# Performance work log

Hardware: AMD Instinct MI355X
Metric: run time of the kernel (lower is better)

The kernel has to match this reference:

```python
import jax, jax.numpy as jnp
import numpy as np
import math

D = 2048
N1 = 250  # fixed by fc1 = Linear(250, 1)
N2 = 27   # fixed by fc2 = Linear(27, 1) for img_size=96


def setup_inputs() -> dict:
    key = jax.random.key(0)
    ks = jax.random.split(key, 18)
    s = 0.02
    def w(k, shape):
        return jax.random.normal(k, shape, dtype=jnp.float32) * s
    return {
        "input_tensor1": jax.random.normal(ks[0], (N1, D), dtype=jnp.float32),
        "input_tensor2": jax.random.normal(ks[1], (N2, D), dtype=jnp.float32),
        "Wq1": w(ks[2], (D, D)), "bq1": jnp.zeros((D,), jnp.float32),
        "Wk1": w(ks[3], (D, D)), "bk1": jnp.zeros((D,), jnp.float32),
        "Wv1": w(ks[4], (D, D)), "bv1": jnp.zeros((D,), jnp.float32),
        "Wq2": w(ks[5], (D, D)), "bq2": jnp.zeros((D,), jnp.float32),
        "Wk2": w(ks[6], (D, D)), "bk2": jnp.zeros((D,), jnp.float32),
        "Wv2": w(ks[7], (D, D)), "bv2": jnp.zeros((D,), jnp.float32),
        "w_fc1": w(ks[8], (N1,)), "b_fc1": jnp.zeros((), jnp.float32),
        "w_fc2": w(ks[9], (N2,)), "b_fc2": jnp.zeros((), jnp.float32),
    }


def reference(input_tensor1, input_tensor2,
              Wq1, bq1, Wk1, bk1, Wv1, bv1,
              Wq2, bq2, Wk2, bk2, Wv2, bv2,
              w_fc1, b_fc1, w_fc2, b_fc2):
    d = input_tensor1.shape[1]
    q1 = input_tensor1 @ Wq1.T + bq1  # [N1, D]
    k1 = input_tensor1 @ Wk1.T + bk1
    v1 = input_tensor1 @ Wv1.T + bv1
    q2 = input_tensor2 @ Wq2.T + bq2  # [N2, D]
    k2 = input_tensor2 @ Wk2.T + bk2
    v2 = input_tensor2 @ Wv2.T + bv2
    scale = 1.0 / math.sqrt(d)

    # sigmoid cross-attention scores
    probs1 = jax.nn.sigmoid((q2 @ k1.T) * scale)  # [N2, N1]
    probs2 = jax.nn.sigmoid((q1 @ k2.T) * scale)  # [N1, N2]

    # Original builds whole[t, i, d] = probs1[t, i] * v2[t, d] then applies
    # fc1 (Linear(N1,1)) along i: ctx1[t,d] = v2[t,d] * (probs1[t,:] @ w_fc1) + b_fc1.
    # Fused form avoids the [N2, N1, D] intermediate; math identical.
    context_layer1 = v2 * (probs1 @ w_fc1)[:, None] + b_fc1  # [N2, D]
    context_layer2 = v1 * (probs2 @ w_fc2)[:, None] + b_fc2  # [N1, D]

    return (context_layer2, probs2, context_layer1, probs1)
```

## Files before the change

kernel.cpp:

```cpp
#include <hip/hip_runtime.h>

typedef unsigned short u16;
typedef unsigned int u32;
typedef __attribute__((ext_vector_type(8))) short short8;
typedef __attribute__((ext_vector_type(4))) float f32x4;

#define DD 2048
constexpr int OFF_P2   = 512000;
constexpr int OFF_CTX1 = 518750;
constexpr int OFF_P1   = 574046;

constexpr int SLB = 512000;
constexpr int SLS = 55296;
constexpr int Q1P = 0;
constexpr int K1P = 1024000;
constexpr int V1P = 2048000;
constexpr int Q2P = 3072000;
constexpr int K2P = Q2P + 4*SLS;
constexpr int V2P = K2P + 4*SLS;
constexpr int S1P = V2P + 4*SLS;
constexpr int S2P = S1P + 8*8192;
constexpr int G1A = S2P + 8*8192;

__device__ __forceinline__ u16 f2bf(float f){
  u32 u = __float_as_uint(f);
  u += 0x7fffu + ((u >> 16) & 1u);
  return (u16)(u >> 16);
}
__device__ __forceinline__ u32 pk(float a, float b){
  return (u32)f2bf(a) | ((u32)f2bf(b) << 16);
}

struct P6 { const float* W[6]; const float* b[6]; };

__global__ __launch_bounds__(256) void k6nt(
    const float* __restrict__ in1, const float* __restrict__ in2,
    P6 par, float* __restrict__ ws)
{
  __shared__ u16 lds_a[64*72];
  __shared__ u16 lds_b[64*72];
  const int b = blockIdx.x, t = threadIdx.x;
  const float* A; int Mreal, m0, n0, kbase, KT, g; float* outp;
  if (b < 768){
    g = b >> 8; int r = b & 255;
    m0 = (r >> 6) * 64; int r2 = r & 63; n0 = (r2 >> 1) * 64; int ks = r2 & 1;
    A = in1; Mreal = 250; kbase = ks * 1024; KT = 16;
    outp = ws + g * (2*SLB) + ks * SLB;
  } else {
    int s = b - 768; g = 3 + s / 128; int r = s % 128;
    n0 = (r >> 2) * 64; int ks = r & 3;
    A = in2; Mreal = 27; m0 = 0; kbase = ks * 512; KT = 8;
    outp = ws + Q2P + (g - 3) * (4*SLS) + ks * SLS;
  }
  const bool addb = (kbase == 0);
  const float* Bw = par.W[g];
  const float* bias = par.b[g];

  const int w = t>>6, l = t&63, wm = w>>1, wn = w&1;
  const int srow = t>>4, scol = (t&15)*4;
  float4 pfa[4], pfb[4];

  auto loadt = [&](int k0){
#pragma unroll
    for (int p=0;p<4;p++){
      int row = p*16 + srow;
      int gm = m0 + row;
      if (gm < Mreal) pfa[p] = *(const float4*)&A[(size_t)gm*DD + k0 + scol];
      else { pfa[p].x=0.f; pfa[p].y=0.f; pfa[p].z=0.f; pfa[p].w=0.f; }
      pfb[p] = *(const float4*)&Bw[(size_t)(n0+row)*DD + k0 + scol];
    }
  };

  f32x4 acc[2][2];
#pragma unroll
  for (int i=0;i<2;i++)
#pragma unroll
    for (int j=0;j<2;j++) acc[i][j] = (f32x4){0.f,0.f,0.f,0.f};

  loadt(kbase);
#pragma unroll 1
  for (int kt=0; kt<KT; ++kt){
    __syncthreads();
#pragma unroll
    for (int p=0;p<4;p++){
      int row = p*16 + srow;
      uint2 av; av.x = pk(pfa[p].x, pfa[p].y); av.y = pk(pfa[p].z, pfa[p].w);
      *(uint2*)&lds_a[row*72 + scol] = av;
      uint2 bw; bw.x = pk(pfb[p].x, pfb[p].y); bw.y = pk(pfb[p].z, pfb[p].w);
      *(uint2*)&lds_b[row*72 + scol] = bw;
    }
    __syncthreads();
    if (kt < KT-1) loadt(kbase + (kt+1)*64);
#pragma unroll
    for (int kk=0; kk<2; ++kk){
      const int kf = kk*32 + (l>>4)*8;
      short8 af[2], bfr[2];
#pragma unroll
      for (int mf=0;mf<2;mf++) af[mf]  = *(const short8*)&lds_a[(wm*32+mf*16+(l&15))*72 + kf];
#pragma unroll
      for (int nf=0;nf<2;nf++) bfr[nf] = *(const short8*)&lds_b[(wn*32+nf*16+(l&15))*72 + kf];
#pragma unroll
      for (int mf=0;mf<2;mf++)
#pragma unroll
        for (int nf=0;nf<2;nf++)
          acc[mf][nf] = __builtin_amdgcn_mfma_f32_16x16x32_bf16(af[mf], bfr[nf], acc[mf][nf], 0, 0, 0);
    }
  }
#pragma unroll
  for (int mf=0;mf<2;mf++)
#pragma unroll
    for (int nf=0;nf<2;nf++){
      int colg = n0 + wn*32 + nf*16 + (l&15);
      float bv = addb ? bias[colg] : 0.f;
#pragma unroll
      for (int r=0;r<4;r++){
        int m = m0 + wm*32 + mf*16 + ((l>>4)<<2) + r;
        if (m < Mreal) outp[(size_t)m*DD + colg] = acc[mf][nf][r] + bv;
      }
    }
}

__global__ __launch_bounds__(256) void kS(float* __restrict__ ws)
{
  __shared__ u16 lds_a[32*72];
  __shared__ u16 lds_b[64*72];
  const int b = blockIdx.x, t = threadIdx.x;
  const int mat = b>>5, r = b&31, jt = r>>3, ks = r&7;
  const int j0 = jt*64, kbase = ks*256;
  const float* Ap = ws + (mat ? K2P : Q2P);
  const float* Bp = ws + (mat ? Q1P : K1P);
  float* OUT = ws + (mat ? S2P : S1P) + ks*8192;
  const int w = t>>6, l = t&63, wm = w>>1, wn = w&1;
  f32x4 acc[2];
  acc[0] = (f32x4){0.f,0.f,0.f,0.f};
  acc[1] = (f32x4){0.f,0.f,0.f,0.f};
#pragma unroll 1
  for (int kt=0; kt<4; ++kt){
    const int kc = kbase + kt*64;
    __syncthreads();
#pragma unroll
    for (int p=0;p<2;p++){
      int f4i = p*256 + t, row = f4i>>4, c4 = (f4i&15)*4;
      float4 v; v.x=0.f; v.y=0.f; v.z=0.f; v.w=0.f;
      if (row < 27){
        const float* base = Ap + (size_t)row*DD + kc + c4;
        float4 v0 = *(const float4*)(base);
        float4 v1 = *(const float4*)(base + SLS);
        float4 v2 = *(const float4*)(base + 2*SLS);
        float4 v3 = *(const float4*)(base + 3*SLS);
        v.x = (v0.x+v1.x)+(v2.x+v3.x); v.y = (v0.y+v1.y)+(v2.y+v3.y);
        v.z = (v0.z+v1.z)+(v2.z+v3.z); v.w = (v0.w+v1.w)+(v2.w+v3.w);
      }
      uint2 pv; pv.x = pk(v.x, v.y); pv.y = pk(v.z, v.w);
      *(uint2*)&lds_a[row*72 + c4] = pv;
    }
#pragma unroll
    for (int p=0;p<4;p++){
      int f4i = p*256 + t, row = f4i>>4, c4 = (f4i&15)*4;
      int j = j0 + row;
      float4 v; v.x=0.f; v.y=0.f; v.z=0.f; v.w=0.f;
      if (j < 250){
        const float* base = Bp + (size_t)j*DD + kc + c4;
        float4 v0 = *(const float4*)(base);
        float4 v1 = *(const float4*)(base + SLB);
        v.x = v0.x+v1.x; v.y = v0.y+v1.y; v.z = v0.z+v1.z; v.w = v0.w+v1.w;
      }
      uint2 pv; pv.x = pk(v.x, v.y); pv.y = pk(v.z, v.w);
      *(uint2*)&lds_b[row*72 + c4] = pv;
    }
    __syncthreads();
#pragma unroll
    for (int kk=0; kk<2; ++kk){
      const int kf = kk*32 + (l>>4)*8;
      short8 af = *(const short8*)&lds_a[(wm*16+(l&15))*72 + kf];
#pragma unroll
      for (int nf=0;nf<2;nf++){
        short8 bfr = *(const short8*)&lds_b[(wn*32+nf*16+(l&15))*72 + kf];
        acc[nf] = __builtin_amdgcn_mfma_f32_16x16x32_bf16(af, bfr, acc[nf], 0, 0, 0);
      }
    }
  }
#pragma unroll
  for (int nf=0;nf<2;nf++){
    int col = j0 + wn*32 + nf*16 + (l&15);
#pragma unroll
    for (int rr=0;rr<4;rr++){
      int row = wm*16 + ((l>>4)<<2) + rr;
      OUT[row*256 + col] = acc[nf][rr];
    }
  }
}

__global__ __launch_bounds__(256) void k_finish(
    const float* __restrict__ ws,
    const float* __restrict__ w_fc1, const float* __restrict__ w_fc2,
    const float* __restrict__ b_fc1p, const float* __restrict__ b_fc2p,
    float* __restrict__ g1acc, float* __restrict__ d_out)
{
  const int b = blockIdx.x, t = threadIdx.x, w = t>>6, l = t&63;
  const int j = b*4 + w;
  if (j >= 250) return;
  const float scale = 0.022097086912079608f;
  float gv = 0.f;
  if (l < 27){
    const float* S1p = ws + S1P;
    const float* S2p = ws + S2P;
    float s1 = 0.f, s2 = 0.f;
#pragma unroll
    for (int p=0;p<8;p++){
      s1 += S1p[p*8192 + l*256 + j];
      s2 += S2p[p*8192 + l*256 + j];
    }
    float p1 = 1.f / (1.f + expf(-s1*scale));
    float p2 = 1.f / (1.f + expf(-s2*scale));
    d_out[OFF_P1 + l*250 + j] = p1;
    d_out[OFF_P2 + j*27 + l] = p2;
    atomicAdd(&g1acc[l], p1 * w_fc1[j]);
    gv = p2 * w_fc2[l];
  }
#pragma unroll
  for (int off=32; off; off>>=1) gv += __shfl_xor(gv, off);
  const float g2 = gv, bfc2 = b_fc2p[0];
  const float* v1a = ws + V1P;
  const float* v1b = ws + V1P + SLB;
#pragma unroll
  for (int i=0;i<8;i++){
    int e4 = (l + 64*i)*4;
    float4 va = *(const float4*)&v1a[(size_t)j*DD + e4];
    float4 vb = *(const float4*)&v1b[(size_t)j*DD + e4];
    float4 o;
    o.x = (va.x+vb.x)*g2 + bfc2; o.y = (va.y+vb.y)*g2 + bfc2;
    o.z = (va.z+vb.z)*g2 + bfc2; o.w = (va.w+vb.w)*g2 + bfc2;
    *(float4*)&d_out[(size_t)j*DD + e4] = o;
  }
}

__global__ __launch_bounds__(256) void k_ctx1(
    const float* __restrict__ ws, const float* __restrict__ g1acc,
    const float* __restrict__ b_fc1p, float* __restrict__ d_out)
{
  const int i = blockIdx.x*256 + threadIdx.x;
  if (i >= 27*512) return;
  const int row = i >> 9, c4 = (i & 511)*4;
  const float* v2p = ws + V2P;
  const float* base = v2p + (size_t)row*DD + c4;
  float4 v0 = *(const float4*)(base);
  float4 v1 = *(const float4*)(base + SLS);
  float4 v2 = *(const float4*)(base + 2*SLS);
  float4 v3 = *(const float4*)(base + 3*SLS);
  const float g = g1acc[row], bb = b_fc1p[0];
  float4 o;
  o.x = ((v0.x+v1.x)+(v2.x+v3.x))*g + bb;
  o.y = ((v0.y+v1.y)+(v2.y+v3.y))*g + bb;
  o.z = ((v0.z+v1.z)+(v2.z+v3.z))*g + bb;
  o.w = ((v0.w+v1.w)+(v2.w+v3.w))*g + bb;
  *(float4*)&d_out[OFF_CTX1 + (size_t)row*DD + c4] = o;
}

extern "C" void kernel_launch(void* const* d_in, const int* in_sizes, int n_in,
                              void* d_out, int out_size, void* d_ws, size_t ws_size,
                              hipStream_t stream)
{
  const float* in1 = (const float*)d_in[0];
  const float* in2 = (const float*)d_in[1];
  P6 par;
  par.W[0] = (const float*)d_in[2];  par.b[0] = (const float*)d_in[3];
  par.W[1] = (const float*)d_in[4];  par.b[1] = (const float*)d_in[5];
  par.W[2] = (const float*)d_in[6];  par.b[2] = (const float*)d_in[7];
  par.W[3] = (const float*)d_in[8];  par.b[3] = (const float*)d_in[9];
  par.W[4] = (const float*)d_in[10]; par.b[4] = (const float*)d_in[11];
  par.W[5] = (const float*)d_in[12]; par.b[5] = (const float*)d_in[13];
  const float* wfc1 = (const float*)d_in[14]; const float* bfc1 = (const float*)d_in[15];
  const float* wfc2 = (const float*)d_in[16]; const float* bfc2 = (const float*)d_in[17];
  float* out = (float*)d_out;
  float* ws  = (float*)d_ws;
  float* g1acc = ws + G1A;

  hipMemsetAsync(g1acc, 0, 32*sizeof(float), stream);
  k6nt<<<1152, 256, 0, stream>>>(in1, in2, par, ws);
  kS<<<64, 256, 0, stream>>>(ws);
  k_finish<<<63, 256, 0, stream>>>(ws, wfc1, wfc2, bfc1, bfc2, g1acc, out);
  k_ctx1<<<54, 256, 0, stream>>>(ws, g1acc, bfc1, out);
}
```

Measured before the change: 205.8 us.

## Replace LDS-tiled GEMMs with register-direct MFMA GEMMs and drop split-K for N1

```diff
diff --git a/kernel.cpp b/kernel.cpp
--- a/kernel.cpp
+++ b/kernel.cpp
@@ -1,4 +1,5 @@
 #include <hip/hip_runtime.h>
+#include <hip/hip_bf16.h>
 
 typedef unsigned short u16;
 typedef unsigned int u32;
@@ -10,185 +11,148 @@
 constexpr int OFF_CTX1 = 518750;
 constexpr int OFF_P1   = 574046;
 
-constexpr int SLB = 512000;
-constexpr int SLS = 55296;
-constexpr int Q1P = 0;
-constexpr int K1P = 1024000;
-constexpr int V1P = 2048000;
-constexpr int Q2P = 3072000;
-constexpr int K2P = Q2P + 4*SLS;
-constexpr int V2P = K2P + 4*SLS;
-constexpr int S1P = V2P + 4*SLS;
-constexpr int S2P = S1P + 8*8192;
-constexpr int G1A = S2P + 8*8192;
-
-__device__ __forceinline__ u16 f2bf(float f){
-  u32 u = __float_as_uint(f);
-  u += 0x7fffu + ((u >> 16) & 1u);
-  return (u16)(u >> 16);
-}
-__device__ __forceinline__ u32 pk(float a, float b){
-  return (u32)f2bf(a) | ((u32)f2bf(b) << 16);
+constexpr int Q1S = 0;
+constexpr int K1S = 524288;
+constexpr int V1S = 1048576;
+constexpr int SMP = 1572864;
+constexpr int S1P = 2359296;
+constexpr int S2P = 2424832;
+constexpr int G1A = 2490368;
+
+__device__ __forceinline__ u32 pk2(float a, float b){
+  __hip_bfloat162 h = __float22bfloat162_rn(make_float2(a, b));
+  u32 r; __builtin_memcpy(&r, &h, 4); return r;
+}
+__device__ __forceinline__ short8 cvt8(float4 u, float4 v, bool ok){
+  union { short8 s; u32 w[4]; } r;
+  r.w[0] = ok ? pk2(u.x,u.y) : 0u;
+  r.w[1] = ok ? pk2(u.z,u.w) : 0u;
+  r.w[2] = ok ? pk2(v.x,v.y) : 0u;
+  r.w[3] = ok ? pk2(v.z,v.w) : 0u;
+  return r.s;
+}
+
+template<int MF, int NF, int KST, int NP>
+__device__ __forceinline__ void gemm_reg(
+    const float* __restrict__ A, int Aslice,
+    int mbase, int Mclamp,
+    const float* __restrict__ W, int nbase, int kbase,
+    const float* __restrict__ bias, bool addb,
+    float* __restrict__ outp, int ldo, int obase_m, int obase_n, int lane)
+{
+  const int lr = lane & 15, lk8 = (lane >> 4) * 8;
+  const float* ap[MF]; bool aok[MF];
+#pragma unroll
+  for (int mf=0; mf<MF; ++mf){
+    int gm = mbase + mf*16 + lr;
+    aok[mf] = gm < Mclamp;
+    int cg = aok[mf] ? gm : (Mclamp-1);
+    ap[mf] = A + (size_t)cg*DD + kbase + lk8;
+  }
+  const float* bp[NF];
+#pragma unroll
+  for (int nf=0; nf<NF; ++nf)
+    bp[nf] = W + (size_t)(nbase + nf*16 + lr)*DD + kbase + lk8;
+
+  f32x4 acc[MF][NF];
+#pragma unroll
+  for (int i=0;i<MF;i++)
+#pragma unroll
+    for (int j=0;j<NF;j++) acc[i][j] = (f32x4){0.f,0.f,0.f,0.f};
+
+  float4 ax[MF][NP][2], bx[NF][2];
+  float4 ay[MF][NP][2], by[NF][2];
+
+  auto issue = [&](int ks, float4 (&am)[MF][NP][2], float4 (&bm)[NF][2]){
+    const int off = ks*32;
+#pragma unroll
+    for (int mf=0; mf<MF; ++mf)
+#pragma unroll
+      for (int p=0; p<NP; ++p){
+        am[mf][p][0] = *(const float4*)(ap[mf] + (size_t)p*Aslice + off);
+        am[mf][p][1] = *(const float4*)(ap[mf] + (size_t)p*Aslice + off + 4);
+      }
+#pragma unroll
+    for (int nf=0; nf<NF; ++nf){
+      bm[nf][0] = *(const float4*)(bp[nf] + off);
+      bm[nf][1] = *(const float4*)(bp[nf] + off + 4);
+    }
+  };
+  auto comp = [&](float4 (&am)[MF][NP][2], float4 (&bm)[NF][2]){
+    short8 af[MF], bf[NF];
+#pragma unroll
+    for (int mf=0; mf<MF; ++mf){
+      float4 u = am[mf][0][0], v = am[mf][0][1];
+#pragma unroll
+      for (int p=1; p<NP; ++p){ u += am[mf][p][0]; v += am[mf][p][1]; }
+      af[mf] = cvt8(u, v, aok[mf]);
+    }
+#pragma unroll
+    for (int nf=0; nf<NF; ++nf) bf[nf] = cvt8(bm[nf][0], bm[nf][1], true);
+#pragma unroll
+    for (int mf=0; mf<MF; ++mf)
+#pragma unroll
+      for (int nf=0; nf<NF; ++nf)
+        acc[mf][nf] = __builtin_amdgcn_mfma_f32_16x16x32_bf16(af[mf], bf[nf], acc[mf][nf], 0,0,0);
+  };
+
+  issue(0, ax, bx);
+#pragma unroll 1
+  for (int ks=0; ks<KST; ks+=2){
+    issue(ks+1, ay, by);
+    comp(ax, bx);
+    issue(ks+2 < KST ? ks+2 : 0, ax, bx);
+    comp(ay, by);
+  }
+
+  const int lq = (lane>>4)*4;
+#pragma unroll
+  for (int mf=0; mf<MF; ++mf)
+#pragma unroll
+    for (int nf=0; nf<NF; ++nf){
+      int col = obase_n + nf*16 + lr;
+      float bv = addb ? bias[col] : 0.f;
+#pragma unroll
+      for (int rr=0; rr<4; ++rr){
+        int row = obase_m + mf*16 + lq + rr;
+        outp[(size_t)row*ldo + col] = acc[mf][nf][rr] + bv;
+      }
+    }
 }
 
 struct P6 { const float* W[6]; const float* b[6]; };
 
-__global__ __launch_bounds__(256) void k6nt(
-    const float* __restrict__ in1, const float* __restrict__ in2,
-    P6 par, float* __restrict__ ws)
-{
-  __shared__ u16 lds_a[64*72];
-  __shared__ u16 lds_b[64*72];
-  const int b = blockIdx.x, t = threadIdx.x;
-  const float* A; int Mreal, m0, n0, kbase, KT, g; float* outp;
-  if (b < 768){
-    g = b >> 8; int r = b & 255;
-    m0 = (r >> 6) * 64; int r2 = r & 63; n0 = (r2 >> 1) * 64; int ks = r2 & 1;
-    A = in1; Mreal = 250; kbase = ks * 1024; KT = 16;
-    outp = ws + g * (2*SLB) + ks * SLB;
+__global__ __launch_bounds__(256) void kA(const float* __restrict__ in1,
+                                          const float* __restrict__ in2,
+                                          P6 par, float* __restrict__ ws)
+{
+  const int b = blockIdx.x, t = threadIdx.x, l = t&63, w = t>>6;
+  if (b < 192){
+    const int mat = b>>6, r = b&63, mt = r>>5, nt = r&31;
+    const int wm = w>>1, wn = w&1;
+    const int mbase = mt*128 + wm*64, nbase = nt*64 + wn*32;
+    gemm_reg<4,2,64,1>(in1, 0, mbase, 250, par.W[mat], nbase, 0,
+                       par.b[mat], true, ws + (size_t)mat*524288, DD, mbase, nbase, l);
   } else {
-    int s = b - 768; g = 3 + s / 128; int r = s % 128;
-    n0 = (r >> 2) * 64; int ks = r & 3;
-    A = in2; Mreal = 27; m0 = 0; kbase = ks * 512; KT = 8;
-    outp = ws + Q2P + (g - 3) * (4*SLS) + ks * SLS;
-  }
-  const bool addb = (kbase == 0);
-  const float* Bw = par.W[g];
-  const float* bias = par.b[g];
-
-  const int w = t>>6, l = t&63, wm = w>>1, wn = w&1;
-  const int srow = t>>4, scol = (t&15)*4;
-  float4 pfa[4], pfb[4];
-
-  auto loadt = [&](int k0){
-#pragma unroll
-    for (int p=0;p<4;p++){
-      int row = p*16 + srow;
-      int gm = m0 + row;
-      if (gm < Mreal) pfa[p] = *(const float4*)&A[(size_t)gm*DD + k0 + scol];
-      else { pfa[p].x=0.f; pfa[p].y=0.f; pfa[p].z=0.f; pfa[p].w=0.f; }
-      pfb[p] = *(const float4*)&Bw[(size_t)(n0+row)*DD + k0 + scol];
-    }
-  };
-
-  f32x4 acc[2][2];
-#pragma unroll
-  for (int i=0;i<2;i++)
-#pragma unroll
-    for (int j=0;j<2;j++) acc[i][j] = (f32x4){0.f,0.f,0.f,0.f};
-
-  loadt(kbase);
-#pragma unroll 1
-  for (int kt=0; kt<KT; ++kt){
-    __syncthreads();
-#pragma unroll
-    for (int p=0;p<4;p++){
-      int row = p*16 + srow;
-      uint2 av; av.x = pk(pfa[p].x, pfa[p].y); av.y = pk(pfa[p].z, pfa[p].w);
-      *(uint2*)&lds_a[row*72 + scol] = av;
-      uint2 bw; bw.x = pk(pfb[p].x, pfb[p].y); bw.y = pk(pfb[p].z, pfb[p].w);
-      *(uint2*)&lds_b[row*72 + scol] = bw;
-    }
-    __syncthreads();
-    if (kt < KT-1) loadt(kbase + (kt+1)*64);
-#pragma unroll
-    for (int kk=0; kk<2; ++kk){
-      const int kf = kk*32 + (l>>4)*8;
-      short8 af[2], bfr[2];
-#pragma unroll
-      for (int mf=0;mf<2;mf++) af[mf]  = *(const short8*)&lds_a[(wm*32+mf*16+(l&15))*72 + kf];
-#pragma unroll
-      for (int nf=0;nf<2;nf++) bfr[nf] = *(const short8*)&lds_b[(wn*32+nf*16+(l&15))*72 + kf];
-#pragma unroll
-      for (int mf=0;mf<2;mf++)
-#pragma unroll
-        for (int nf=0;nf<2;nf++)
-          acc[mf][nf] = __builtin_amdgcn_mfma_f32_16x16x32_bf16(af[mf], bfr[nf], acc[mf][nf], 0, 0, 0);
-    }
-  }
-#pragma unroll
-  for (int mf=0;mf<2;mf++)
-#pragma unroll
-    for (int nf=0;nf<2;nf++){
-      int colg = n0 + wn*32 + nf*16 + (l&15);
-      float bv = addb ? bias[colg] : 0.f;
-#pragma unroll
-      for (int r=0;r<4;r++){
-        int m = m0 + wm*32 + mf*16 + ((l>>4)<<2) + r;
-        if (m < Mreal) outp[(size_t)m*DD + colg] = acc[mf][nf][r] + bv;
-      }
-    }
+    const int s = b - 192, mat = s>>5, r = s&31, nt = r>>2, ksp = r&3;
+    const int nbase = nt*256 + w*64;
+    gemm_reg<2,4,16,1>(in2, 0, 0, 27, par.W[3+mat], nbase, ksp*512,
+                       par.b[3+mat], ksp==0,
+                       ws + SMP + (size_t)(mat*4+ksp)*65536, DD, 0, nbase, l);
+  }
 }
 
 __global__ __launch_bounds__(256) void kS(float* __restrict__ ws)
 {
-  __shared__ u16 lds_a[32*72];
-  __shared__ u16 lds_b[64*72];
-  const int b = blockIdx.x, t = threadIdx.x;
-  const int mat = b>>5, r = b&31, jt = r>>3, ks = r&7;
-  const int j0 = jt*64, kbase = ks*256;
-  const float* Ap = ws + (mat ? K2P : Q2P);
-  const float* Bp = ws + (mat ? Q1P : K1P);
-  float* OUT = ws + (mat ? S2P : S1P) + ks*8192;
-  const int w = t>>6, l = t&63, wm = w>>1, wn = w&1;
-  f32x4 acc[2];
-  acc[0] = (f32x4){0.f,0.f,0.f,0.f};
-  acc[1] = (f32x4){0.f,0.f,0.f,0.f};
-#pragma unroll 1
-  for (int kt=0; kt<4; ++kt){
-    const int kc = kbase + kt*64;
-    __syncthreads();
-#pragma unroll
-    for (int p=0;p<2;p++){
-      int f4i = p*256 + t, row = f4i>>4, c4 = (f4i&15)*4;
-      float4 v; v.x=0.f; v.y=0.f; v.z=0.f; v.w=0.f;
-      if (row < 27){
-        const float* base = Ap + (size_t)row*DD + kc + c4;
-        float4 v0 = *(const float4*)(base);
-        float4 v1 = *(const float4*)(base + SLS);
-        float4 v2 = *(const float4*)(base + 2*SLS);
-        float4 v3 = *(const float4*)(base + 3*SLS);
-        v.x = (v0.x+v1.x)+(v2.x+v3.x); v.y = (v0.y+v1.y)+(v2.y+v3.y);
-        v.z = (v0.z+v1.z)+(v2.z+v3.z); v.w = (v0.w+v1.w)+(v2.w+v3.w);
-      }
-      uint2 pv; pv.x = pk(v.x, v.y); pv.y = pk(v.z, v.w);
-      *(uint2*)&lds_a[row*72 + c4] = pv;
-    }
-#pragma unroll
-    for (int p=0;p<4;p++){
-      int f4i = p*256 + t, row = f4i>>4, c4 = (f4i&15)*4;
-      int j = j0 + row;
-      float4 v; v.x=0.f; v.y=0.f; v.z=0.f; v.w=0.f;
-      if (j < 250){
-        const float* base = Bp + (size_t)j*DD + kc + c4;
-        float4 v0 = *(const float4*)(base);
-        float4 v1 = *(const float4*)(base + SLB);
-        v.x = v0.x+v1.x; v.y = v0.y+v1.y; v.z = v0.z+v1.z; v.w = v0.w+v1.w;
-      }
-      uint2 pv; pv.x = pk(v.x, v.y); pv.y = pk(v.z, v.w);
-      *(uint2*)&lds_b[row*72 + c4] = pv;
-    }
-    __syncthreads();
-#pragma unroll
-    for (int kk=0; kk<2; ++kk){
-      const int kf = kk*32 + (l>>4)*8;
-      short8 af = *(const short8*)&lds_a[(wm*16+(l&15))*72 + kf];
-#pragma unroll
-      for (int nf=0;nf<2;nf++){
-        short8 bfr = *(const short8*)&lds_b[(wn*32+nf*16+(l&15))*72 + kf];
-        acc[nf] = __builtin_amdgcn_mfma_f32_16x16x32_bf16(af, bfr, acc[nf], 0, 0, 0);
-      }
-    }
-  }
-#pragma unroll
-  for (int nf=0;nf<2;nf++){
-    int col = j0 + wn*32 + nf*16 + (l&15);
-#pragma unroll
-    for (int rr=0;rr<4;rr++){
-      int row = wm*16 + ((l>>4)<<2) + rr;
-      OUT[row*256 + col] = acc[nf][rr];
-    }
-  }
+  const int b = blockIdx.x, t = threadIdx.x, l = t&63, w = t>>6;
+  if (b == 0 && t < 32) ws[G1A + t] = 0.f;
+  const int mat = b>>4, r = b&15, jt = r>>3, ksp = r&7;
+  const float* Ab = ws + SMP + (size_t)mat*4*65536;
+  const float* Bb = ws + (mat ? Q1S : K1S);
+  float* OUT = ws + (mat ? S2P : S1P) + ksp*8192;
+  const int jbase = jt*128 + w*32;
+  gemm_reg<2,2,8,4>(Ab, 65536, 0, 32, Bb, jbase, ksp*256,
+                    nullptr, false, OUT, 256, 0, jbase, l);
 }
 
 __global__ __launch_bounds__(256) void k_finish(
@@ -197,63 +161,63 @@
     const float* __restrict__ b_fc1p, const float* __restrict__ b_fc2p,
     float* __restrict__ g1acc, float* __restrict__ d_out)
 {
-  const int b = blockIdx.x, t = threadIdx.x, w = t>>6, l = t&63;
-  const int j = b*4 + w;
-  if (j >= 250) return;
-  const float scale = 0.022097086912079608f;
-  float gv = 0.f;
-  if (l < 27){
-    const float* S1p = ws + S1P;
-    const float* S2p = ws + S2P;
-    float s1 = 0.f, s2 = 0.f;
-#pragma unroll
-    for (int p=0;p<8;p++){
-      s1 += S1p[p*8192 + l*256 + j];
-      s2 += S2p[p*8192 + l*256 + j];
-    }
-    float p1 = 1.f / (1.f + expf(-s1*scale));
-    float p2 = 1.f / (1.f + expf(-s2*scale));
-    d_out[OFF_P1 + l*250 + j] = p1;
-    d_out[OFF_P2 + j*27 + l] = p2;
-    atomicAdd(&g1acc[l], p1 * w_fc1[j]);
-    gv = p2 * w_fc2[l];
-  }
-#pragma unroll
-  for (int off=32; off; off>>=1) gv += __shfl_xor(gv, off);
-  const float g2 = gv, bfc2 = b_fc2p[0];
-  const float* v1a = ws + V1P;
-  const float* v1b = ws + V1P + SLB;
-#pragma unroll
-  for (int i=0;i<8;i++){
-    int e4 = (l + 64*i)*4;
-    float4 va = *(const float4*)&v1a[(size_t)j*DD + e4];
-    float4 vb = *(const float4*)&v1b[(size_t)j*DD + e4];
+  const int j = blockIdx.x, t = threadIdx.x, l = t&63, w = t>>6;
+  __shared__ float g2s;
+  if (w == 0){
+    const float scale = 0.022097086912079608f;
+    float gv = 0.f;
+    if (l < 27){
+      const float* S1p = ws + S1P;
+      const float* S2p = ws + S2P;
+      float s1 = 0.f, s2 = 0.f;
+#pragma unroll
+      for (int p=0;p<8;p++){
+        s1 += S1p[p*8192 + l*256 + j];
+        s2 += S2p[p*8192 + l*256 + j];
+      }
+      float p1 = 1.f / (1.f + expf(-s1*scale));
+      float p2 = 1.f / (1.f + expf(-s2*scale));
+      d_out[OFF_P1 + l*250 + j] = p1;
+      d_out[OFF_P2 + j*27 + l] = p2;
+      atomicAdd(&g1acc[l], p1 * w_fc1[j]);
+      gv = p2 * w_fc2[l];
+    }
+#pragma unroll
+    for (int off=32; off; off>>=1) gv += __shfl_xor(gv, off);
+    if (l == 0) g2s = gv;
+  }
+  __syncthreads();
+  const float g2 = g2s, bfc2 = b_fc2p[0];
+  const float* v1 = ws + V1S + (size_t)j*DD;
+#pragma unroll
+  for (int i=0;i<2;i++){
+    int e = (t + 256*i)*4;
+    float4 v = *(const float4*)&v1[e];
     float4 o;
-    o.x = (va.x+vb.x)*g2 + bfc2; o.y = (va.y+vb.y)*g2 + bfc2;
-    o.z = (va.z+vb.z)*g2 + bfc2; o.w = (va.w+vb.w)*g2 + bfc2;
-    *(float4*)&d_out[(size_t)j*DD + e4] = o;
+    o.x = v.x*g2 + bfc2; o.y = v.y*g2 + bfc2;
+    o.z = v.z*g2 + bfc2; o.w = v.w*g2 + bfc2;
+    *(float4*)&d_out[(size_t)j*DD + e] = o;
   }
 }
 
 __global__ __launch_bounds__(256) void k_ctx1(
-    const float* __restrict__ ws, const float* __restrict__ g1acc,
-    const float* __restrict__ b_fc1p, float* __restrict__ d_out)
+    const float* __restrict__ ws, const float* __restrict__ b_fc1p,
+    float* __restrict__ d_out)
 {
   const int i = blockIdx.x*256 + threadIdx.x;
   if (i >= 27*512) return;
   const int row = i >> 9, c4 = (i & 511)*4;
-  const float* v2p = ws + V2P;
-  const float* base = v2p + (size_t)row*DD + c4;
-  float4 v0 = *(const float4*)(base);
-  float4 v1 = *(const float4*)(base + SLS);
-  float4 v2 = *(const float4*)(base + 2*SLS);
-  float4 v3 = *(const float4*)(base + 3*SLS);
-  const float g = g1acc[row], bb = b_fc1p[0];
+  const float* v2 = ws + SMP + (size_t)8*65536 + (size_t)row*DD + c4;
+  float4 v0 = *(const float4*)(v2);
+  float4 v1 = *(const float4*)(v2 + 65536);
+  float4 v2b = *(const float4*)(v2 + 2*65536);
+  float4 v3 = *(const float4*)(v2 + 3*65536);
+  const float g = ws[G1A + row], bb = b_fc1p[0];
   float4 o;
-  o.x = ((v0.x+v1.x)+(v2.x+v3.x))*g + bb;
-  o.y = ((v0.y+v1.y)+(v2.y+v3.y))*g + bb;
-  o.z = ((v0.z+v1.z)+(v2.z+v3.z))*g + bb;
-  o.w = ((v0.w+v1.w)+(v2.w+v3.w))*g + bb;
+  o.x = ((v0.x+v1.x)+(v2b.x+v3.x))*g + bb;
+  o.y = ((v0.y+v1.y)+(v2b.y+v3.y))*g + bb;
+  o.z = ((v0.z+v1.z)+(v2b.z+v3.z))*g + bb;
+  o.w = ((v0.w+v1.w)+(v2b.w+v3.w))*g + bb;
   *(float4*)&d_out[OFF_CTX1 + (size_t)row*DD + c4] = o;
 }
 
@@ -274,11 +238,9 @@
   const float* wfc2 = (const float*)d_in[16]; const float* bfc2 = (const float*)d_in[17];
   float* out = (float*)d_out;
   float* ws  = (float*)d_ws;
-  float* g1acc = ws + G1A;
-
-  hipMemsetAsync(g1acc, 0, 32*sizeof(float), stream);
-  k6nt<<<1152, 256, 0, stream>>>(in1, in2, par, ws);
-  kS<<<64, 256, 0, stream>>>(ws);
-  k_finish<<<63, 256, 0, stream>>>(ws, wfc1, wfc2, bfc1, bfc2, g1acc, out);
-  k_ctx1<<<54, 256, 0, stream>>>(ws, g1acc, bfc1, out);
-}
+
+  kA<<<288, 256, 0, stream>>>(in1, in2, par, ws);
+  kS<<<32, 256, 0, stream>>>(ws);
+  k_finish<<<250, 256, 0, stream>>>(ws, wfc1, wfc2, bfc1, bfc2, ws + G1A, out);
+  k_ctx1<<<54, 256, 0, stream>>>(ws, bfc1, out);
+}
```

After: 370.4 us. +80.0%, slower.
